# Kernel optimization log

Hardware: AMD Instinct MI355X
Metric: run time of the kernel (lower is better)

The kernel has to match this reference:

```python
import jax, jax.numpy as jnp
import numpy as np

B, C, F = 262144, 64, 256
N_ITERS = 8


def setup_inputs() -> dict:
    key = jax.random.key(0)
    ks = jax.random.split(key, 8)
    s = lambda fan_in: 1.0 / np.sqrt(fan_in)
    return {
        "y": jax.random.normal(ks[0], (B, C), jnp.float32),
        "log_det_jacobians": jnp.zeros((B,), jnp.float32),
        "v": jax.random.normal(ks[1], (B, 1, C), jnp.float32),
        "W1": jax.random.normal(ks[2], (F, C), jnp.float32) * s(C),
        "b1": jnp.zeros((F,), jnp.float32),
        "W2": jax.random.normal(ks[3], (F, F), jnp.float32) * s(F),
        "b2": jnp.zeros((F,), jnp.float32),
        "W3": jax.random.normal(ks[4], (C, F), jnp.float32) * s(F),
        "b3": jnp.zeros((C,), jnp.float32),
    }


def reference(y, log_det_jacobians, v, W1, b1, W2, b2, W3, b3):
    def mlp(t):
        h = jax.nn.elu(t)
        h = jax.nn.elu(h @ W1.T + b1)
        h = jax.nn.elu(h @ W2.T + b2)
        return h @ W3.T + b3  # [B, C]

    g_y, vjp_fn = jax.vjp(mlp, y)
    v0 = v[:, 0, :]  # n_samples = 1
    w = v0
    log_det = jnp.zeros((y.shape[0],), y.dtype)
    for k in range(1, N_ITERS + 1):
        w = vjp_fn(w)[0]              # w <- w @ J, J = dg/dy
        inner = jnp.einsum('bd,bd->b', w, v0)
        # torch code: add when (k+1) % 2 == 0 (k odd), subtract when k even
        log_det = log_det + (inner / k if (k + 1) % 2 == 0 else -inner / k)

    z = y + g_y
    return z, log_det_jacobians + log_det
```

## Files before the change

kernel.cpp:

```cpp
#include <hip/hip_runtime.h>

#define BN 262144

typedef short bf16x8 __attribute__((ext_vector_type(8)));
typedef float f32x4 __attribute__((ext_vector_type(4)));
typedef unsigned int u32x2 __attribute__((ext_vector_type(2)));

#define MFMA16(a,b,c) __builtin_amdgcn_mfma_f32_16x16x32_bf16((a),(b),(c),0,0,0)

__device__ __forceinline__ unsigned short f2bf(float f) {
  union { float f; unsigned int u; } x; x.f = f;
  unsigned int u = x.u + 0x7fffu + ((x.u >> 16) & 1u);
  return (unsigned short)(u >> 16);
}
__device__ __forceinline__ float bf2f(unsigned int h) {
  union { unsigned int u; float f; } x; x.u = h << 16;
  return x.f;
}
__device__ __forceinline__ unsigned short tbf(float f) {
  union { float f; unsigned int u; } x; x.f = f;
  return (unsigned short)(x.u >> 16);
}
__device__ __forceinline__ unsigned pk2(float lo, float hi) {
  union { float f; unsigned int u; } a, b; a.f = lo; b.f = hi;
  return (a.u >> 16) | (b.u & 0xffff0000u);
}
__device__ __forceinline__ unsigned swz(int row) {
  return (((unsigned)(row & 7)) << 4) ^ (((unsigned)(row & 8)) << 2);
}

#define O_R1 0
#define O_R2 16384
#define O_R3 81920
#define O_R4 98304
#define O_R5 114688
#define O_R6 180224
#define N_WS 196608

__global__ void invres_prep(const float* __restrict__ W1, const float* __restrict__ W2,
                            const float* __restrict__ W3, unsigned short* __restrict__ wsb) {
  int idx = blockIdx.x * 256 + threadIdx.x;
  if (idx >= N_WS) return;
  int j = idx & 7;
  int lane = (idx >> 3) & 63;
  int nn = lane & 15, kn = (lane >> 4) * 8 + j;
  float val;
  if (idx < O_R2) {
    int g = idx >> 9; int s = g & 1; int ct = g >> 1;
    val = W1[(ct * 16 + nn) * 64 + (s * 32 + kn)];
  } else if (idx < O_R3) {
    int g = (idx - O_R2) >> 9; int s = g & 7; int ct = g >> 3;
    val = W2[(ct * 16 + nn) * 256 + (s * 32 + kn)];
  } else if (idx < O_R4) {
    int g = (idx - O_R3) >> 9; int s = g & 7; int ct = g >> 3;
    val = W3[(ct * 16 + nn) * 256 + (s * 32 + kn)];
  } else if (idx < O_R5) {
    int g = (idx - O_R4) >> 9; int s = g & 1; int ct = g >> 1;
    val = W3[(s * 32 + kn) * 256 + (ct * 16 + nn)];
  } else if (idx < O_R6) {
    int g = (idx - O_R5) >> 9; int s = g & 7; int ct = g >> 3;
    val = W2[(s * 32 + kn) * 256 + (ct * 16 + nn)];
  } else {
    int g = (idx - O_R6) >> 9; int s = g & 7; int ct = g >> 3;
    val = W1[(s * 32 + kn) * 64 + (ct * 16 + nn)];
  }
  wsb[idx] = f2bf(val);
}

#define L_PB  16384
#define L_WB  32768
#define L_D1  36864
#define L_D2  53248
#define L_LDP 69632
#define L_SIZE 70144

__global__ void __launch_bounds__(512, 4)
invres_main(const float* __restrict__ y, const float* __restrict__ ldj,
            const float* __restrict__ v, const float* __restrict__ b1,
            const float* __restrict__ b2, const float* __restrict__ b3,
            const unsigned short* __restrict__ wsb, float* __restrict__ out) {
  extern __shared__ char smem[];
  char* PA = smem;
  char* PB = smem + L_PB;
  char* WB = smem + L_WB;
  char* D1 = smem + L_D1;
  char* D2 = smem + L_D2;
  float* ldp = (float*)(smem + L_LDP);

  const int tid = threadIdx.x;
  const int lane = tid & 63;
  const int wid = tid >> 6;
  const int l15 = lane & 15, g16 = lane >> 4;
  const int ct0 = wid * 2;
  const int mh = wid >> 2;
  const int ctn = wid & 3;
  const int r0 = blockIdx.x * 32;

  const bf16x8* R1 = (const bf16x8*)(wsb + O_R1);
  const bf16x8* R2 = (const bf16x8*)(wsb + O_R2);
  const bf16x8* R3 = (const bf16x8*)(wsb + O_R3);
  const bf16x8* R4 = (const bf16x8*)(wsb + O_R4);
  const bf16x8* R5 = (const bf16x8*)(wsb + O_R5);
  const bf16x8* R6 = (const bf16x8*)(wsb + O_R6);

  auto mOff = [&](int mc) -> int { return ((wid * 4 + mc) * 64 + lane) * 8; };

  auto ldsA = [&](const char* buf, int mm, int s) -> bf16x8 {
    int row = mm * 16 + l15;
    unsigned byte = ((unsigned)(s * 64 + g16 * 16)) ^ swz(row);
    return *(const bf16x8*)(buf + row * 512 + byte);
  };
  auto dstoreW = [&](char* buf, int mm, int cc, int r, float val) {
    int row = mm * 16 + g16 * 4 + r;
    int col = (ct0 + cc) * 16 + l15;
    *(unsigned short*)(buf + row * 512 + (((unsigned)(col * 2)) ^ swz(row))) = tbf(val);
  };
  auto gA = [&](const float* p, int mm, int s, bool elu) -> bf16x8 {
    const float* q = p + (size_t)(r0 + mm * 16 + l15) * 64 + s * 32 + g16 * 8;
    f32x4 a = __builtin_nontemporal_load((const f32x4*)q);
    f32x4 b = __builtin_nontemporal_load((const f32x4*)(q + 4));
    float xv[8] = {a[0], a[1], a[2], a[3], b[0], b[1], b[2], b[3]};
    bf16x8 f;
#pragma unroll
    for (int i = 0; i < 8; i++) {
      float x = xv[i];
      if (elu) x = x > 0.f ? x : (__expf(x) - 1.f);
      f[i] = (short)f2bf(x);
    }
    return f;
  };

  float bb1[2], bb2[2];
#pragma unroll
  for (int cc = 0; cc < 2; cc++) {
    bb1[cc] = b1[(ct0 + cc) * 16 + l15];
    bb2[cc] = b2[(ct0 + cc) * 16 + l15];
  }
  const float bb3 = b3[ctn * 16 + l15];

  unsigned d0p[2], v0p[2];
  float ldacc[4] = {0.f, 0.f, 0.f, 0.f};

  {
    f32x4 acc[2][2] = {};
#pragma unroll
    for (int s = 0; s < 2; s++) {
      bf16x8 a0 = gA(y, 0, s, true);
      bf16x8 a1 = gA(y, 1, s, true);
#pragma unroll
      for (int cc = 0; cc < 2; cc++) {
        bf16x8 B = R1[((ct0 + cc) * 2 + s) * 64 + lane];
        acc[0][cc] = MFMA16(a0, B, acc[0][cc]);
        acc[1][cc] = MFMA16(a1, B, acc[1][cc]);
      }
    }
#pragma unroll
    for (int mm = 0; mm < 2; mm++)
#pragma unroll
      for (int cc = 0; cc < 2; cc++) {
        float dv[4];
#pragma unroll
        for (int r = 0; r < 4; r++) {
          float a = acc[mm][cc][r] + bb1[cc];
          float e = __expf(a);
          float h = a > 0.f ? a : (e - 1.f);
          dv[r] = a > 0.f ? 1.f : e;
          dstoreW(PA, mm, cc, r, h);
        }
        u32x2 w; w[0] = pk2(dv[0], dv[1]); w[1] = pk2(dv[2], dv[3]);
        *(u32x2*)(D1 + mOff(mm * 2 + cc)) = w;
      }
  }
  __syncthreads();

  {
    f32x4 acc[2][2] = {};
    bf16x8 a0 = ldsA(PA, 0, 0);
    bf16x8 a1 = ldsA(PA, 1, 0);
#pragma unroll 1
    for (int s = 0; s < 8; s++) {
      bf16x8 c0 = a0, c1 = a1;
      int sn = s < 7 ? s + 1 : 7;
      a0 = ldsA(PA, 0, sn);
      a1 = ldsA(PA, 1, sn);
      bf16x8 B0 = R2[(ct0 * 8 + s) * 64 + lane];
      bf16x8 B1 = R2[((ct0 + 1) * 8 + s) * 64 + lane];
      acc[0][0] = MFMA16(c0, B0, acc[0][0]);
      acc[0][1] = MFMA16(c0, B1, acc[0][1]);
      acc[1][0] = MFMA16(c1, B0, acc[1][0]);
      acc[1][1] = MFMA16(c1, B1, acc[1][1]);
    }
#pragma unroll
    for (int mm = 0; mm < 2; mm++)
#pragma unroll
      for (int cc = 0; cc < 2; cc++) {
        float dv[4];
#pragma unroll
        for (int r = 0; r < 4; r++) {
          float a = acc[mm][cc][r] + bb2[cc];
          float e = __expf(a);
          float h = a > 0.f ? a : (e - 1.f);
          dv[r] = a > 0.f ? 1.f : e;
          dstoreW(PB, mm, cc, r, h);
        }
        u32x2 w; w[0] = pk2(dv[0], dv[1]); w[1] = pk2(dv[2], dv[3]);
        *(u32x2*)(D2 + mOff(mm * 2 + cc)) = w;
      }
  }
  __syncthreads();

  {
    f32x4 acc0 = {}, acc1 = {};
    bf16x8 p0 = ldsA(PB, mh, 0);
    bf16x8 p1 = ldsA(PB, mh, 1);
#pragma unroll 1
    for (int s = 0; s < 8; s += 2) {
      bf16x8 c0 = p0, c1 = p1;
      int sn = s + 2 < 8 ? s + 2 : 0;
      p0 = ldsA(PB, mh, sn);
      p1 = ldsA(PB, mh, sn + 1);
      acc0 = MFMA16(c0, R3[(ctn * 8 + s) * 64 + lane], acc0);
      acc1 = MFMA16(c1, R3[(ctn * 8 + s + 1) * 64 + lane], acc1);
    }
    float d0v[4], v0v[4];
#pragma unroll
    for (int r = 0; r < 4; r++) {
      float av = acc0[r] + acc1[r];
      int row = r0 + mh * 16 + g16 * 4 + r;
      int col = ctn * 16 + l15;
      size_t off = (size_t)row * 64 + col;
      float yv = __builtin_nontemporal_load(y + off);
      __builtin_nontemporal_store(yv + av + bb3, out + off);
      d0v[r] = yv > 0.f ? 1.f : __expf(yv);
      v0v[r] = __builtin_nontemporal_load(v + off);
    }
    d0p[0] = pk2(d0v[0], d0v[1]); d0p[1] = pk2(d0v[2], d0v[3]);
    v0p[0] = pk2(v0v[0], v0v[1]); v0p[1] = pk2(v0v[2], v0v[3]);
  }

  {
    f32x4 acc[2][2] = {};
#pragma unroll
    for (int s = 0; s < 2; s++) {
      bf16x8 a0 = gA(v, 0, s, false);
      bf16x8 a1 = gA(v, 1, s, false);
#pragma unroll
      for (int cc = 0; cc < 2; cc++) {
        bf16x8 B = R4[((ct0 + cc) * 2 + s) * 64 + lane];
        acc[0][cc] = MFMA16(a0, B, acc[0][cc]);
        acc[1][cc] = MFMA16(a1, B, acc[1][cc]);
      }
    }
#pragma unroll
    for (int mm = 0; mm < 2; mm++)
#pragma unroll
      for (int cc = 0; cc < 2; cc++) {
        u32x2 dd = *(const u32x2*)(D2 + mOff(mm * 2 + cc));
#pragma unroll
        for (int r = 0; r < 4; r++) {
          float u = acc[mm][cc][r] * bf2f((dd[r >> 1] >> ((r & 1) * 16)) & 0xffffu);
          dstoreW(PA, mm, cc, r, u);
        }
      }
  }
  __syncthreads();

  for (int k = 1; k <= 8; ++k) {
    {
      f32x4 acc[2][2] = {};
      bf16x8 a0 = ldsA(PA, 0, 0);
      bf16x8 a1 = ldsA(PA, 1, 0);
#pragma unroll 1
      for (int s = 0; s < 8; s++) {
        bf16x8 c0 = a0, c1 = a1;
        int sn = s < 7 ? s + 1 : 7;
        a0 = ldsA(PA, 0, sn);
        a1 = ldsA(PA, 1, sn);
        bf16x8 B0 = R5[(ct0 * 8 + s) * 64 + lane];
        bf16x8 B1 = R5[((ct0 + 1) * 8 + s) * 64 + lane];
        acc[0][0] = MFMA16(c0, B0, acc[0][0]);
        acc[0][1] = MFMA16(c0, B1, acc[0][1]);
        acc[1][0] = MFMA16(c1, B0, acc[1][0]);
        acc[1][1] = MFMA16(c1, B1, acc[1][1]);
      }
#pragma unroll
      for (int mm = 0; mm < 2; mm++)
#pragma unroll
        for (int cc = 0; cc < 2; cc++) {
          u32x2 dd = *(const u32x2*)(D1 + mOff(mm * 2 + cc));
#pragma unroll
          for (int r = 0; r < 4; r++) {
            float u = acc[mm][cc][r] * bf2f((dd[r >> 1] >> ((r & 1) * 16)) & 0xffffu);
            dstoreW(PB, mm, cc, r, u);
          }
        }
    }
    __syncthreads();

    {
      float coef = (k & 1) ? (1.f / (float)k) : (-1.f / (float)k);
      f32x4 acc0 = {}, acc1 = {};
      bf16x8 p0 = ldsA(PB, mh, 0);
      bf16x8 p1 = ldsA(PB, mh, 1);
#pragma unroll 1
      for (int s = 0; s < 8; s += 2) {
        bf16x8 c0 = p0, c1 = p1;
        int sn = s + 2 < 8 ? s + 2 : 0;
        p0 = ldsA(PB, mh, sn);
        p1 = ldsA(PB, mh, sn + 1);
        acc0 = MFMA16(c0, R6[(ctn * 8 + s) * 64 + lane], acc0);
        acc1 = MFMA16(c1, R6[(ctn * 8 + s + 1) * 64 + lane], acc1);
      }
#pragma unroll
      for (int r = 0; r < 4; r++) {
        float wv = (acc0[r] + acc1[r]) * bf2f((d0p[r >> 1] >> ((r & 1) * 16)) & 0xffffu);
        ldacc[r] += coef * wv * bf2f((v0p[r >> 1] >> ((r & 1) * 16)) & 0xffffu);
        if (k < 8) {
          int row = mh * 16 + g16 * 4 + r;
          int col = ctn * 16 + l15;
          *(unsigned short*)(WB + row * 128 + (((unsigned)(col * 2)) ^ swz(row))) = tbf(wv);
        }
      }
    }
    if (k < 8) {
      __syncthreads();
      f32x4 acc[2][2] = {};
#pragma unroll
      for (int s = 0; s < 2; s++) {
        bf16x8 a0, a1;
#pragma unroll
        for (int mm = 0; mm < 2; mm++) {
          int row = mm * 16 + l15;
          unsigned byte = ((unsigned)(s * 64 + g16 * 16)) ^ swz(row);
          bf16x8 a = *(const bf16x8*)(WB + row * 128 + byte);
          if (mm == 0) a0 = a; else a1 = a;
        }
#pragma unroll
        for (int cc = 0; cc < 2; cc++) {
          bf16x8 B = R4[((ct0 + cc) * 2 + s) * 64 + lane];
          acc[0][cc] = MFMA16(a0, B, acc[0][cc]);
          acc[1][cc] = MFMA16(a1, B, acc[1][cc]);
        }
      }
#pragma unroll
      for (int mm = 0; mm < 2; mm++)
#pragma unroll
        for (int cc = 0; cc < 2; cc++) {
          u32x2 dd = *(const u32x2*)(D2 + mOff(mm * 2 + cc));
#pragma unroll
          for (int r = 0; r < 4; r++) {
            float u = acc[mm][cc][r] * bf2f((dd[r >> 1] >> ((r & 1) * 16)) & 0xffffu);
            dstoreW(PA, mm, cc, r, u);
          }
        }
      __syncthreads();
    }
  }

#pragma unroll
  for (int r = 0; r < 4; r++) {
    float s = ldacc[r];
    s += __shfl_xor(s, 1);
    s += __shfl_xor(s, 2);
    s += __shfl_xor(s, 4);
    s += __shfl_xor(s, 8);
    ldacc[r] = s;
  }
  if (l15 == 0) {
#pragma unroll
    for (int r = 0; r < 4; r++) {
      int row = mh * 16 + g16 * 4 + r;
      ldp[row * 4 + ctn] = ldacc[r];
    }
  }
  __syncthreads();
  if (tid < 32) {
    float s = ldp[tid * 4] + ldp[tid * 4 + 1] + ldp[tid * 4 + 2] + ldp[tid * 4 + 3];
    int gb = r0 + tid;
    __builtin_nontemporal_store(ldj[gb] + s, out + (size_t)BN * 64 + gb);
  }
}

extern "C" void kernel_launch(void* const* d_in, const int* in_sizes, int n_in,
                              void* d_out, int out_size, void* d_ws, size_t ws_size,
                              hipStream_t stream) {
  const float* y   = (const float*)d_in[0];
  const float* ldj = (const float*)d_in[1];
  const float* v   = (const float*)d_in[2];
  const float* W1  = (const float*)d_in[3];
  const float* b1  = (const float*)d_in[4];
  const float* W2  = (const float*)d_in[5];
  const float* b2  = (const float*)d_in[6];
  const float* W3  = (const float*)d_in[7];
  const float* b3  = (const float*)d_in[8];
  unsigned short* wsb = (unsigned short*)d_ws;
  float* out = (float*)d_out;

  (void)hipFuncSetAttribute(reinterpret_cast<const void*>(&invres_main),
                            hipFuncAttributeMaxDynamicSharedMemorySize, L_SIZE);

  invres_prep<<<N_WS / 256, 256, 0, stream>>>(W1, W2, W3, wsb);
  invres_main<<<BN / 32, 512, L_SIZE, stream>>>(y, ldj, v, b1, b2, b3, wsb, out);
}
```

Before: 813.8 us.

## Swap MFMA operands to transpose accumulators and vectorize LDS and global stores

Swaps the A/B operands of every MFMA so each lane's accumulator holds four consecutive columns of one row instead of four rows of one column. This lets intermediate activations be written to LDS as packed 8-byte stores rather than scalar 2-byte stores. The y/v loads and the z store become 16-byte vector accesses, and bias loads become vectors. The final log-det reduction is simplified to an in-lane sum plus two cross-group shuffles. The aim is fewer LDS store instructions, fewer bank-conflicted narrow writes and fewer global memory transactions, at the cost of reworked index math that must keep the swizzle consistent.

```diff
diff --git a/kernel.cpp b/kernel.cpp
--- a/kernel.cpp
+++ b/kernel.cpp
@@ -16,10 +16,6 @@
 __device__ __forceinline__ float bf2f(unsigned int h) {
   union { unsigned int u; float f; } x; x.u = h << 16;
   return x.f;
-}
-__device__ __forceinline__ unsigned short tbf(float f) {
-  union { float f; unsigned int u; } x; x.f = f;
-  return (unsigned short)(x.u >> 16);
 }
 __device__ __forceinline__ unsigned pk2(float lo, float hi) {
   union { float f; unsigned int u; } a, b; a.f = lo; b.f = hi;
@@ -110,10 +106,11 @@
     unsigned byte = ((unsigned)(s * 64 + g16 * 16)) ^ swz(row);
     return *(const bf16x8*)(buf + row * 512 + byte);
   };
-  auto dstoreW = [&](char* buf, int mm, int cc, int r, float val) {
-    int row = mm * 16 + g16 * 4 + r;
-    int col = (ct0 + cc) * 16 + l15;
-    *(unsigned short*)(buf + row * 512 + (((unsigned)(col * 2)) ^ swz(row))) = tbf(val);
+  auto stage64 = [&](char* buf, int mm, int cc, const float* hv) {
+    int row = mm * 16 + l15;
+    unsigned byte = ((unsigned)(((ct0 + cc) * 16 + g16 * 4) * 2)) ^ swz(row);
+    u32x2 w; w[0] = pk2(hv[0], hv[1]); w[1] = pk2(hv[2], hv[3]);
+    *(u32x2*)(buf + row * 512 + byte) = w;
   };
   auto gA = [&](const float* p, int mm, int s, bool elu) -> bf16x8 {
     const float* q = p + (size_t)(r0 + mm * 16 + l15) * 64 + s * 32 + g16 * 8;
@@ -130,13 +127,13 @@
     return f;
   };
 
-  float bb1[2], bb2[2];
+  f32x4 bv1[2], bv2[2], bv3;
 #pragma unroll
   for (int cc = 0; cc < 2; cc++) {
-    bb1[cc] = b1[(ct0 + cc) * 16 + l15];
-    bb2[cc] = b2[(ct0 + cc) * 16 + l15];
-  }
-  const float bb3 = b3[ctn * 16 + l15];
+    bv1[cc] = *(const f32x4*)(b1 + (ct0 + cc) * 16 + g16 * 4);
+    bv2[cc] = *(const f32x4*)(b2 + (ct0 + cc) * 16 + g16 * 4);
+  }
+  bv3 = *(const f32x4*)(b3 + ctn * 16 + g16 * 4);
 
   unsigned d0p[2], v0p[2];
   float ldacc[4] = {0.f, 0.f, 0.f, 0.f};
@@ -150,23 +147,23 @@
 #pragma unroll
       for (int cc = 0; cc < 2; cc++) {
         bf16x8 B = R1[((ct0 + cc) * 2 + s) * 64 + lane];
-        acc[0][cc] = MFMA16(a0, B, acc[0][cc]);
-        acc[1][cc] = MFMA16(a1, B, acc[1][cc]);
+        acc[0][cc] = MFMA16(B, a0, acc[0][cc]);
+        acc[1][cc] = MFMA16(B, a1, acc[1][cc]);
       }
     }
 #pragma unroll
     for (int mm = 0; mm < 2; mm++)
 #pragma unroll
       for (int cc = 0; cc < 2; cc++) {
-        float dv[4];
+        float hv[4], dv[4];
 #pragma unroll
         for (int r = 0; r < 4; r++) {
-          float a = acc[mm][cc][r] + bb1[cc];
+          float a = acc[mm][cc][r] + bv1[cc][r];
           float e = __expf(a);
-          float h = a > 0.f ? a : (e - 1.f);
+          hv[r] = a > 0.f ? a : (e - 1.f);
           dv[r] = a > 0.f ? 1.f : e;
-          dstoreW(PA, mm, cc, r, h);
-        }
+        }
+        stage64(PA, mm, cc, hv);
         u32x2 w; w[0] = pk2(dv[0], dv[1]); w[1] = pk2(dv[2], dv[3]);
         *(u32x2*)(D1 + mOff(mm * 2 + cc)) = w;
       }
@@ -185,24 +182,24 @@
       a1 = ldsA(PA, 1, sn);
       bf16x8 B0 = R2[(ct0 * 8 + s) * 64 + lane];
       bf16x8 B1 = R2[((ct0 + 1) * 8 + s) * 64 + lane];
-      acc[0][0] = MFMA16(c0, B0, acc[0][0]);
-      acc[0][1] = MFMA16(c0, B1, acc[0][1]);
-      acc[1][0] = MFMA16(c1, B0, acc[1][0]);
-      acc[1][1] = MFMA16(c1, B1, acc[1][1]);
+      acc[0][0] = MFMA16(B0, c0, acc[0][0]);
+      acc[0][1] = MFMA16(B1, c0, acc[0][1]);
+      acc[1][0] = MFMA16(B0, c1, acc[1][0]);
+      acc[1][1] = MFMA16(B1, c1, acc[1][1]);
     }
 #pragma unroll
     for (int mm = 0; mm < 2; mm++)
 #pragma unroll
       for (int cc = 0; cc < 2; cc++) {
-        float dv[4];
+        float hv[4], dv[4];
 #pragma unroll
         for (int r = 0; r < 4; r++) {
-          float a = acc[mm][cc][r] + bb2[cc];
+          float a = acc[mm][cc][r] + bv2[cc][r];
           float e = __expf(a);
-          float h = a > 0.f ? a : (e - 1.f);
+          hv[r] = a > 0.f ? a : (e - 1.f);
           dv[r] = a > 0.f ? 1.f : e;
-          dstoreW(PB, mm, cc, r, h);
-        }
+        }
+        stage64(PB, mm, cc, hv);
         u32x2 w; w[0] = pk2(dv[0], dv[1]); w[1] = pk2(dv[2], dv[3]);
         *(u32x2*)(D2 + mOff(mm * 2 + cc)) = w;
       }
@@ -219,23 +216,24 @@
       int sn = s + 2 < 8 ? s + 2 : 0;
       p0 = ldsA(PB, mh, sn);
       p1 = ldsA(PB, mh, sn + 1);
-      acc0 = MFMA16(c0, R3[(ctn * 8 + s) * 64 + lane], acc0);
-      acc1 = MFMA16(c1, R3[(ctn * 8 + s + 1) * 64 + lane], acc1);
-    }
-    float d0v[4], v0v[4];
+      acc0 = MFMA16(R3[(ctn * 8 + s) * 64 + lane], c0, acc0);
+      acc1 = MFMA16(R3[(ctn * 8 + s + 1) * 64 + lane], c1, acc1);
+    }
+    int row = r0 + mh * 16 + l15;
+    int col = ctn * 16 + g16 * 4;
+    size_t off = (size_t)row * 64 + col;
+    f32x4 yv = __builtin_nontemporal_load((const f32x4*)(y + off));
+    f32x4 vv = __builtin_nontemporal_load((const f32x4*)(v + off));
+    f32x4 zv;
+    float d0v[4];
 #pragma unroll
     for (int r = 0; r < 4; r++) {
-      float av = acc0[r] + acc1[r];
-      int row = r0 + mh * 16 + g16 * 4 + r;
-      int col = ctn * 16 + l15;
-      size_t off = (size_t)row * 64 + col;
-      float yv = __builtin_nontemporal_load(y + off);
-      __builtin_nontemporal_store(yv + av + bb3, out + off);
-      d0v[r] = yv > 0.f ? 1.f : __expf(yv);
-      v0v[r] = __builtin_nontemporal_load(v + off);
-    }
+      zv[r] = yv[r] + acc0[r] + acc1[r] + bv3[r];
+      d0v[r] = yv[r] > 0.f ? 1.f : __expf(yv[r]);
+    }
+    __builtin_nontemporal_store(zv, (f32x4*)(out + off));
     d0p[0] = pk2(d0v[0], d0v[1]); d0p[1] = pk2(d0v[2], d0v[3]);
-    v0p[0] = pk2(v0v[0], v0v[1]); v0p[1] = pk2(v0v[2], v0v[3]);
+    v0p[0] = pk2(vv[0], vv[1]);   v0p[1] = pk2(vv[2], vv[3]);
   }
 
   {
@@ -247,8 +245,8 @@
 #pragma unroll
       for (int cc = 0; cc < 2; cc++) {
         bf16x8 B = R4[((ct0 + cc) * 2 + s) * 64 + lane];
-        acc[0][cc] = MFMA16(a0, B, acc[0][cc]);
-        acc[1][cc] = MFMA16(a1, B, acc[1][cc]);
+        acc[0][cc] = MFMA16(B, a0, acc[0][cc]);
+        acc[1][cc] = MFMA16(B, a1, acc[1][cc]);
       }
     }
 #pragma unroll
@@ -256,11 +254,11 @@
 #pragma unroll
       for (int cc = 0; cc < 2; cc++) {
         u32x2 dd = *(const u32x2*)(D2 + mOff(mm * 2 + cc));
-#pragma unroll
-        for (int r = 0; r < 4; r++) {
-          float u = acc[mm][cc][r] * bf2f((dd[r >> 1] >> ((r & 1) * 16)) & 0xffffu);
-          dstoreW(PA, mm, cc, r, u);
-        }
+        float uv[4];
+#pragma unroll
+        for (int r = 0; r < 4; r++)
+          uv[r] = acc[mm][cc][r] * bf2f((dd[r >> 1] >> ((r & 1) * 16)) & 0xffffu);
+        stage64(PA, mm, cc, uv);
       }
   }
   __syncthreads();
@@ -278,21 +276,21 @@
         a1 = ldsA(PA, 1, sn);
         bf16x8 B0 = R5[(ct0 * 8 + s) * 64 + lane];
         bf16x8 B1 = R5[((ct0 + 1) * 8 + s) * 64 + lane];
-        acc[0][0] = MFMA16(c0, B0, acc[0][0]);
-        acc[0][1] = MFMA16(c0, B1, acc[0][1]);
-        acc[1][0] = MFMA16(c1, B0, acc[1][0]);
-        acc[1][1] = MFMA16(c1, B1, acc[1][1]);
+        acc[0][0] = MFMA16(B0, c0, acc[0][0]);
+        acc[0][1] = MFMA16(B1, c0, acc[0][1]);
+        acc[1][0] = MFMA16(B0, c1, acc[1][0]);
+        acc[1][1] = MFMA16(B1, c1, acc[1][1]);
       }
 #pragma unroll
       for (int mm = 0; mm < 2; mm++)
 #pragma unroll
         for (int cc = 0; cc < 2; cc++) {
           u32x2 dd = *(const u32x2*)(D1 + mOff(mm * 2 + cc));
-#pragma unroll
-          for (int r = 0; r < 4; r++) {
-            float u = acc[mm][cc][r] * bf2f((dd[r >> 1] >> ((r & 1) * 16)) & 0xffffu);
-            dstoreW(PB, mm, cc, r, u);
-          }
+          float uv[4];
+#pragma unroll
+          for (int r = 0; r < 4; r++)
+            uv[r] = acc[mm][cc][r] * bf2f((dd[r >> 1] >> ((r & 1) * 16)) & 0xffffu);
+          stage64(PB, mm, cc, uv);
         }
     }
     __syncthreads();
@@ -308,18 +306,20 @@
         int sn = s + 2 < 8 ? s + 2 : 0;
         p0 = ldsA(PB, mh, sn);
         p1 = ldsA(PB, mh, sn + 1);
-        acc0 = MFMA16(c0, R6[(ctn * 8 + s) * 64 + lane], acc0);
-        acc1 = MFMA16(c1, R6[(ctn * 8 + s + 1) * 64 + lane], acc1);
-      }
+        acc0 = MFMA16(R6[(ctn * 8 + s) * 64 + lane], c0, acc0);
+        acc1 = MFMA16(R6[(ctn * 8 + s + 1) * 64 + lane], c1, acc1);
+      }
+      float wv[4];
 #pragma unroll
       for (int r = 0; r < 4; r++) {
-        float wv = (acc0[r] + acc1[r]) * bf2f((d0p[r >> 1] >> ((r & 1) * 16)) & 0xffffu);
-        ldacc[r] += coef * wv * bf2f((v0p[r >> 1] >> ((r & 1) * 16)) & 0xffffu);
-        if (k < 8) {
-          int row = mh * 16 + g16 * 4 + r;
-          int col = ctn * 16 + l15;
-          *(unsigned short*)(WB + row * 128 + (((unsigned)(col * 2)) ^ swz(row))) = tbf(wv);
-        }
+        wv[r] = (acc0[r] + acc1[r]) * bf2f((d0p[r >> 1] >> ((r & 1) * 16)) & 0xffffu);
+        ldacc[r] += coef * wv[r] * bf2f((v0p[r >> 1] >> ((r & 1) * 16)) & 0xffffu);
+      }
+      if (k < 8) {
+        int row = mh * 16 + l15;
+        unsigned byte = ((unsigned)((ctn * 16 + g16 * 4) * 2)) ^ swz(row);
+        u32x2 w; w[0] = pk2(wv[0], wv[1]); w[1] = pk2(wv[2], wv[3]);
+        *(u32x2*)(WB + row * 128 + byte) = w;
       }
     }
     if (k < 8) {
@@ -338,8 +338,8 @@
 #pragma unroll
         for (int cc = 0; cc < 2; cc++) {
           bf16x8 B = R4[((ct0 + cc) * 2 + s) * 64 + lane];
-          acc[0][cc] = MFMA16(a0, B, acc[0][cc]);
-          acc[1][cc] = MFMA16(a1, B, acc[1][cc]);
+          acc[0][cc] = MFMA16(B, a0, acc[0][cc]);
+          acc[1][cc] = MFMA16(B, a1, acc[1][cc]);
         }
       }
 #pragma unroll
@@ -347,31 +347,21 @@
 #pragma unroll
         for (int cc = 0; cc < 2; cc++) {
           u32x2 dd = *(const u32x2*)(D2 + mOff(mm * 2 + cc));
-#pragma unroll
-          for (int r = 0; r < 4; r++) {
-            float u = acc[mm][cc][r] * bf2f((dd[r >> 1] >> ((r & 1) * 16)) & 0xffffu);
-            dstoreW(PA, mm, cc, r, u);
-          }
+          float uv[4];
+#pragma unroll
+          for (int r = 0; r < 4; r++)
+            uv[r] = acc[mm][cc][r] * bf2f((dd[r >> 1] >> ((r & 1) * 16)) & 0xffffu);
+          stage64(PA, mm, cc, uv);
         }
       __syncthreads();
     }
   }
 
-#pragma unroll
-  for (int r = 0; r < 4; r++) {
-    float s = ldacc[r];
-    s += __shfl_xor(s, 1);
-    s += __shfl_xor(s, 2);
-    s += __shfl_xor(s, 4);
-    s += __shfl_xor(s, 8);
-    ldacc[r] = s;
-  }
-  if (l15 == 0) {
-#pragma unroll
-    for (int r = 0; r < 4; r++) {
-      int row = mh * 16 + g16 * 4 + r;
-      ldp[row * 4 + ctn] = ldacc[r];
-    }
+  {
+    float s = ldacc[0] + ldacc[1] + ldacc[2] + ldacc[3];
+    s += __shfl_xor(s, 16);
+    s += __shfl_xor(s, 32);
+    if (g16 == 0) ldp[(mh * 16 + l15) * 4 + ctn] = s;
   }
   __syncthreads();
   if (tid < 32) {
```

New measurement: 806.4 us. No clear change (-0.9%).
